# Kernel tuning notes

Measured on AMD Instinct MI355X. Metric: run time of the kernel, lower is better.

## Reference

```python
import jax, jax.numpy as jnp
import numpy as np

HID = 256
POS_FREQ = 10
DIR_FREQ = 4
POS_ENC = 3 * (2 * POS_FREQ + 1)   # 63
DIR_ENC = 3 * (2 * DIR_FREQ + 1)   # 27
N_PTS = 262144


def _posenc(x, num_freq):
    freqs = (2.0 ** jnp.arange(num_freq)).astype(x.dtype)      # [F]
    xf = x[..., None, :] * freqs[:, None]                       # [..., F, D]
    sc = jnp.stack([jnp.sin(xf), jnp.cos(xf)], axis=-2)         # [..., F, 2, D]
    return jnp.concatenate([x, sc.reshape(*x.shape[:-1], -1)], axis=-1)


def _linear_init(key, fan_in, fan_out):
    kw, kb = jax.random.split(key)
    s = 1.0 / np.sqrt(fan_in)
    W = jax.random.uniform(kw, (fan_in, fan_out), jnp.float32, -s, s)
    b = jax.random.uniform(kb, (fan_out,), jnp.float32, -s, s)
    return W, b


def setup_inputs() -> dict:
    key = jax.random.key(0)
    ks = jax.random.split(key, 16)
    inp = {
        "positions": jax.random.normal(ks[0], (N_PTS, 3), jnp.float32),
        "directions": jax.random.normal(ks[1], (N_PTS, 3), jnp.float32),
    }
    W, b = _linear_init(ks[2], POS_ENC, HID)
    inp["W_in"], inp["b_in"] = W, b
    # 7 hidden layers; layer index 4 takes skip concat (HID + POS_ENC)
    for i in range(7):
        fan_in = HID + POS_ENC if i == 4 else HID
        W, b = _linear_init(ks[3 + i], fan_in, HID)
        inp[f"W_h{i}"], inp[f"b_h{i}"] = W, b
    W, b = _linear_init(ks[10], HID, HID + 1)
    inp["W_out"], inp["b_out"] = W, b
    W, b = _linear_init(ks[11], HID + DIR_ENC, HID // 2)
    inp["W_r1"], inp["b_r1"] = W, b
    W, b = _linear_init(ks[12], HID // 2, 3)
    inp["W_r2"], inp["b_r2"] = W, b
    return inp


def _forward(positions, directions, W_in, b_in, hidden_params, W_out, b_out,
             W_r1, b_r1, W_r2, b_r2):
    pe = _posenc(positions, POS_FREQ)    # [N, 63]
    de = _posenc(directions, DIR_FREQ)   # [N, 27]
    h = jax.nn.relu(pe @ W_in + b_in)    # [N, 256]
    for i, (W, b) in enumerate(hidden_params):
        if i == 4:
            h = jnp.concatenate([h, pe], axis=-1)  # skip connection [N, 319]
        h = jax.nn.relu(h @ W + b)
    out = h @ W_out + b_out                      # [N, 257]
    features = out[..., :HID]                    # [N, 256]
    density = jax.nn.relu(out[..., HID:HID + 1])  # [N, 1]
    rgb_in = jnp.concatenate([features, de], axis=-1)  # [N, 283]
    rgb = jax.nn.sigmoid(jax.nn.relu(rgb_in @ W_r1 + b_r1) @ W_r2 + b_r2)  # [N, 3]
    return rgb, density


def reference(positions, directions, W_in, b_in,
              W_h0, b_h0, W_h1, b_h1, W_h2, b_h2, W_h3, b_h3,
              W_h4, b_h4, W_h5, b_h5, W_h6, b_h6,
              W_out, b_out, W_r1, b_r1, W_r2, b_r2):
    hidden = [(W_h0, b_h0), (W_h1, b_h1), (W_h2, b_h2), (W_h3, b_h3),
              (W_h4, b_h4), (W_h5, b_h5), (W_h6, b_h6)]
    return _forward(positions, directions, W_in, b_in, hidden,
                    W_out, b_out, W_r1, b_r1, W_r2, b_r2)
```

## Files before the change

### kernel.cpp

```cpp
#include <hip/hip_runtime.h>
#include <math.h>

#define NPTS 262144
#define MT 64
#define XS 328
#define NWAVE 8

typedef __attribute__((ext_vector_type(8))) short bf16x8;
typedef __attribute__((ext_vector_type(4))) float f32x4;
typedef __attribute__((ext_vector_type(2))) unsigned int u32x2;

__device__ __forceinline__ short f2bf(float f) {
    union { float f; unsigned u; } v; v.f = f;
    unsigned r = v.u + 0x7fffu + ((v.u >> 16) & 1u);
    return (short)(r >> 16);
}
__device__ __forceinline__ unsigned pk2(float a, float b) {
    return ((unsigned)(unsigned short)f2bf(a)) |
           ((unsigned)(unsigned short)f2bf(b) << 16);
}

#define OFF_IN   0
#define SZ_IN    (64*256)
#define OFF_H0   (OFF_IN + SZ_IN)
#define SZ_H     (256*256)
#define OFF_H1   (OFF_H0 + SZ_H)
#define OFF_H2   (OFF_H1 + SZ_H)
#define OFF_H3   (OFF_H2 + SZ_H)
#define OFF_H4   (OFF_H3 + SZ_H)
#define SZ_H4    (320*256)
#define OFF_H5   (OFF_H4 + SZ_H4)
#define OFF_H6   (OFF_H5 + SZ_H)
#define OFF_OUT  (OFF_H6 + SZ_H)
#define SZ_OUT   (256*272)
#define OFF_R1   (OFF_OUT + SZ_OUT)
#define SZ_R1    (288*128)
#define OFF_R2   (OFF_R1 + SZ_R1)
#define SZ_R2    (128*16)
#define WS_TOTAL (OFF_R2 + SZ_R2)

struct PrepP { const float* W[11]; short* ws; };

__global__ __launch_bounds__(256) void prep_all(PrepP pp) {
    int i = blockIdx.x * 256 + threadIdx.x;
    if (i >= WS_TOTAL) return;
    const int offs[12] = {OFF_IN, OFF_H0, OFF_H1, OFF_H2, OFF_H3, OFF_H4,
                          OFF_H5, OFF_H6, OFF_OUT, OFF_R1, OFF_R2, WS_TOTAL};
    const int Ks[11]  = {63,256,256,256,256,319,256,256,256,283,128};
    const int Ns[11]  = {256,256,256,256,256,256,256,256,257,128,3};
    const int Nps[11] = {256,256,256,256,256,256,256,256,272,128,16};
    int seg = 0;
    while (i >= offs[seg + 1]) seg++;
    int li = i - offs[seg];
    int j = li & 7, L = (li >> 3) & 63, tile = li >> 9;
    int nNt = Nps[seg] >> 4;
    int nt = tile % nNt, kt = tile / nNt;
    int k = kt * 32 + ((L >> 4) << 3) + j;
    int n = nt * 16 + (L & 15);
    float v = (k < Ks[seg] && n < Ns[seg]) ? pp.W[seg][k * Ns[seg] + n] : 0.f;
    pp.ws[i] = f2bf(v);
}

struct Params {
    const float *pos, *dir;
    const float *b_in, *b_h0, *b_h1, *b_h2, *b_h3, *b_h4, *b_h5, *b_h6;
    const float *b_out, *b_r1, *b_r2;
    const short *w;
    float *out;
};

template<int NKT, int NS, int NT, int MODE>
__device__ __forceinline__ void layerT(const short* __restrict__ Wsw,
                                       const float* __restrict__ bias,
                                       short* X, float* dout, int p0,
                                       int wave, int lane) {
    const int l15 = lane & 15, quad = lane >> 4;
    f32x4 acc[NS][4];
#pragma unroll
    for (int s = 0; s < NS; s++)
#pragma unroll
        for (int t = 0; t < 4; t++) acc[s][t] = (f32x4){0.f, 0.f, 0.f, 0.f};
    __syncthreads();
    const short* xb = X + l15 * XS + quad * 8;
    for (int kt = 0; kt < NKT; ++kt) {
        bf16x8 b[4];
#pragma unroll
        for (int t = 0; t < 4; t++)
            b[t] = *(const bf16x8*)(xb + t * 16 * XS + kt * 32);
#pragma unroll
        for (int s = 0; s < NS; s++) {
            const int nt = s * NWAVE + wave;
            if (NS * NWAVE > NT && nt >= NT) break;
            bf16x8 a = *(const bf16x8*)(Wsw + (size_t)((kt * NT + nt) * 64 + lane) * 8);
#pragma unroll
            for (int t = 0; t < 4; t++)
                acc[s][t] = __builtin_amdgcn_mfma_f32_16x16x32_bf16(a, b[t], acc[s][t], 0, 0, 0);
        }
    }
    __syncthreads();
#pragma unroll
    for (int s = 0; s < NS; s++) {
        const int nt = s * NWAVE + wave;
        if (NS * NWAVE > NT && nt >= NT) break;
        if (MODE == 1 && nt == 16) {
            if (quad == 0) {
                const float bv = bias[256];
#pragma unroll
                for (int t = 0; t < 4; t++) {
                    const int m = t * 16 + l15;
                    dout[3 * NPTS + p0 + m] = fmaxf(acc[s][t][0] + bv, 0.f);
                }
            }
        } else {
            const int n0 = nt * 16 + quad * 4;
            const f32x4 bv = *(const f32x4*)(bias + n0);
#pragma unroll
            for (int t = 0; t < 4; t++) {
                const int m = t * 16 + l15;
                float v0 = acc[s][t][0] + bv[0];
                float v1 = acc[s][t][1] + bv[1];
                float v2 = acc[s][t][2] + bv[2];
                float v3 = acc[s][t][3] + bv[3];
                if (MODE == 0) {
                    v0 = fmaxf(v0, 0.f); v1 = fmaxf(v1, 0.f);
                    v2 = fmaxf(v2, 0.f); v3 = fmaxf(v3, 0.f);
                }
                u32x2 w; w[0] = pk2(v0, v1); w[1] = pk2(v2, v3);
                *(u32x2*)(X + m * XS + n0) = w;
            }
        }
    }
}

__global__ __launch_bounds__(512, 6) void nerf_fused(Params P) {
    __shared__ __align__(16) short X[MT * XS];
    __shared__ __align__(16) short DE[MT * 32];
    const int tid = threadIdx.x;
    const int wave = tid >> 6, lane = tid & 63;
    const int p0 = blockIdx.x * MT;

    for (int i = tid; i < MT * 64; i += 512) {
        const int pt = i >> 6, d = i & 63;
        float v = 0.f;
        if (d < 3) v = P.pos[(p0 + pt) * 3 + d];
        else if (d < 63) {
            const int e = d - 3, f = e / 6, r = e % 6;
            const float x = P.pos[(p0 + pt) * 3 + (r % 3)];
            const float xf = x * (float)(1 << f);
            v = (r < 3) ? sinf(xf) : cosf(xf);
        }
        const short bv = f2bf(v);
        X[pt * XS + d] = bv;
        X[pt * XS + 256 + d] = bv;
    }
    for (int i = tid; i < MT * 32; i += 512) {
        const int pt = i >> 5, d = i & 31;
        float v = 0.f;
        if (d < 3) v = P.dir[(p0 + pt) * 3 + d];
        else if (d < 27) {
            const int e = d - 3, f = e / 6, r = e % 6;
            const float x = P.dir[(p0 + pt) * 3 + (r % 3)];
            const float xf = x * (float)(1 << f);
            v = (r < 3) ? sinf(xf) : cosf(xf);
        }
        DE[i] = f2bf(v);
    }

    layerT<2, 2, 16, 0>(P.w + OFF_IN, P.b_in, X, P.out, p0, wave, lane);
    layerT<8, 2, 16, 0>(P.w + OFF_H0, P.b_h0, X, P.out, p0, wave, lane);
    layerT<8, 2, 16, 0>(P.w + OFF_H1, P.b_h1, X, P.out, p0, wave, lane);
    layerT<8, 2, 16, 0>(P.w + OFF_H2, P.b_h2, X, P.out, p0, wave, lane);
    layerT<8, 2, 16, 0>(P.w + OFF_H3, P.b_h3, X, P.out, p0, wave, lane);
    layerT<10, 2, 16, 0>(P.w + OFF_H4, P.b_h4, X, P.out, p0, wave, lane);
    layerT<8, 2, 16, 0>(P.w + OFF_H5, P.b_h5, X, P.out, p0, wave, lane);
    layerT<8, 2, 16, 0>(P.w + OFF_H6, P.b_h6, X, P.out, p0, wave, lane);
    layerT<8, 3, 17, 1>(P.w + OFF_OUT, P.b_out, X, P.out, p0, wave, lane);

    __syncthreads();
    for (int i = tid; i < MT * 32; i += 512) {
        const int pt = i >> 5, d = i & 31;
        X[pt * XS + 256 + d] = DE[i];
    }

    layerT<9, 1, 8, 0>(P.w + OFF_R1, P.b_r1, X, P.out, p0, wave, lane);

    __syncthreads();
    if (wave < 4) {
        const int l15 = lane & 15, quad = lane >> 4;
        f32x4 acc = (f32x4){0.f, 0.f, 0.f, 0.f};
        const short* xb = X + (wave * 16 + l15) * XS + quad * 8;
#pragma unroll
        for (int kt = 0; kt < 4; ++kt) {
            bf16x8 b = *(const bf16x8*)(xb + kt * 32);
            bf16x8 a = *(const bf16x8*)(P.w + OFF_R2 + (size_t)(kt * 64 + lane) * 8);
            acc = __builtin_amdgcn_mfma_f32_16x16x32_bf16(a, b, acc, 0, 0, 0);
        }
        if (quad == 0) {
#pragma unroll
            for (int r = 0; r < 3; r++) {
                const float v = acc[r] + P.b_r2[r];
                P.out[(size_t)(p0 + wave * 16 + l15) * 3 + r] = 1.f / (1.f + expf(-v));
            }
        }
    }
}

extern "C" void kernel_launch(void* const* d_in, const int* in_sizes, int n_in,
                              void* d_out, int out_size, void* d_ws, size_t ws_size,
                              hipStream_t stream) {
    short* ws = (short*)d_ws;

    PrepP pp;
    pp.W[0]  = (const float*)d_in[2];
    pp.W[1]  = (const float*)d_in[4];
    pp.W[2]  = (const float*)d_in[6];
    pp.W[3]  = (const float*)d_in[8];
    pp.W[4]  = (const float*)d_in[10];
    pp.W[5]  = (const float*)d_in[12];
    pp.W[6]  = (const float*)d_in[14];
    pp.W[7]  = (const float*)d_in[16];
    pp.W[8]  = (const float*)d_in[18];
    pp.W[9]  = (const float*)d_in[20];
    pp.W[10] = (const float*)d_in[22];
    pp.ws = ws;
    hipLaunchKernelGGL(prep_all, dim3((WS_TOTAL + 255) / 256), dim3(256), 0, stream, pp);

    Params P;
    P.pos  = (const float*)d_in[0];
    P.dir  = (const float*)d_in[1];
    P.b_in = (const float*)d_in[3];
    P.b_h0 = (const float*)d_in[5];
    P.b_h1 = (const float*)d_in[7];
    P.b_h2 = (const float*)d_in[9];
    P.b_h3 = (const float*)d_in[11];
    P.b_h4 = (const float*)d_in[13];
    P.b_h5 = (const float*)d_in[15];
    P.b_h6 = (const float*)d_in[17];
    P.b_out = (const float*)d_in[19];
    P.b_r1 = (const float*)d_in[21];
    P.b_r2 = (const float*)d_in[23];
    P.w = ws;
    P.out = (float*)d_out;
    hipLaunchKernelGGL(nerf_fused, dim3(NPTS / MT), dim3(512), 0, stream, P);
}
```

Measured before the change: 441.9 us.

## Double point tile to 128 with 16 waves and 2D wave tiling

Each block now handles 128 points with 1024 threads, and each wave owns a 4-column-tile by 2-row-tile block of every layer's output instead of striding over N-tiles. Each weight fragment fetched from global memory is therefore reused across twice as many points. The density column of the output layer moves to a separate small MFMA pass run by the first eight waves. LDS becomes dynamic and grows to about 90 KB, so fewer blocks fit per CU, which lowers occupancy and leaves less latency hiding.

```diff
diff --git a/kernel.cpp b/kernel.cpp
--- a/kernel.cpp
+++ b/kernel.cpp
@@ -2,9 +2,9 @@
 #include <math.h>
 
 #define NPTS 262144
-#define MT 64
+#define MT 128
 #define XS 328
-#define NWAVE 8
+#define NTHREADS 1024
 
 typedef __attribute__((ext_vector_type(8))) short bf16x8;
 typedef __attribute__((ext_vector_type(4))) float f32x4;
@@ -69,77 +69,81 @@
     float *out;
 };
 
-template<int NKT, int NS, int NT, int MODE>
+template<int NKT, int NT, int NS, int TM, int MODE>
 __device__ __forceinline__ void layerT(const short* __restrict__ Wsw,
                                        const float* __restrict__ bias,
                                        short* X, float* dout, int p0,
-                                       int wave, int lane) {
+                                       int ntBase, int mtBase, int wave, int lane) {
     const int l15 = lane & 15, quad = lane >> 4;
-    f32x4 acc[NS][4];
-#pragma unroll
-    for (int s = 0; s < NS; s++)
-#pragma unroll
-        for (int t = 0; t < 4; t++) acc[s][t] = (f32x4){0.f, 0.f, 0.f, 0.f};
     __syncthreads();
     const short* xb = X + l15 * XS + quad * 8;
+
+    if (MODE == 1 && wave < 8) {
+        f32x4 ad = (f32x4){0.f, 0.f, 0.f, 0.f};
+        for (int kt = 0; kt < NKT; ++kt) {
+            bf16x8 b = *(const bf16x8*)(xb + wave * 16 * XS + kt * 32);
+            bf16x8 a = *(const bf16x8*)(Wsw + (size_t)((kt * NT + 16) * 64 + lane) * 8);
+            ad = __builtin_amdgcn_mfma_f32_16x16x32_bf16(a, b, ad, 0, 0, 0);
+        }
+        if (quad == 0)
+            dout[3 * NPTS + p0 + wave * 16 + l15] = fmaxf(ad[0] + bias[256], 0.f);
+    }
+
+    f32x4 acc[NS][TM];
+#pragma unroll
+    for (int s = 0; s < NS; s++)
+#pragma unroll
+        for (int t = 0; t < TM; t++) acc[s][t] = (f32x4){0.f, 0.f, 0.f, 0.f};
+
     for (int kt = 0; kt < NKT; ++kt) {
-        bf16x8 b[4];
-#pragma unroll
-        for (int t = 0; t < 4; t++)
-            b[t] = *(const bf16x8*)(xb + t * 16 * XS + kt * 32);
+        bf16x8 b[TM];
+#pragma unroll
+        for (int t = 0; t < TM; t++)
+            b[t] = *(const bf16x8*)(xb + (mtBase + t) * 16 * XS + kt * 32);
 #pragma unroll
         for (int s = 0; s < NS; s++) {
-            const int nt = s * NWAVE + wave;
-            if (NS * NWAVE > NT && nt >= NT) break;
-            bf16x8 a = *(const bf16x8*)(Wsw + (size_t)((kt * NT + nt) * 64 + lane) * 8);
-#pragma unroll
-            for (int t = 0; t < 4; t++)
+            bf16x8 a = *(const bf16x8*)(Wsw + (size_t)((kt * NT + ntBase + s) * 64 + lane) * 8);
+#pragma unroll
+            for (int t = 0; t < TM; t++)
                 acc[s][t] = __builtin_amdgcn_mfma_f32_16x16x32_bf16(a, b[t], acc[s][t], 0, 0, 0);
         }
     }
     __syncthreads();
 #pragma unroll
     for (int s = 0; s < NS; s++) {
-        const int nt = s * NWAVE + wave;
-        if (NS * NWAVE > NT && nt >= NT) break;
-        if (MODE == 1 && nt == 16) {
-            if (quad == 0) {
-                const float bv = bias[256];
-#pragma unroll
-                for (int t = 0; t < 4; t++) {
-                    const int m = t * 16 + l15;
-                    dout[3 * NPTS + p0 + m] = fmaxf(acc[s][t][0] + bv, 0.f);
-                }
+        const int n0 = (ntBase + s) * 16 + quad * 4;
+        const f32x4 bv = *(const f32x4*)(bias + n0);
+#pragma unroll
+        for (int t = 0; t < TM; t++) {
+            const int m = (mtBase + t) * 16 + l15;
+            float v0 = acc[s][t][0] + bv[0];
+            float v1 = acc[s][t][1] + bv[1];
+            float v2 = acc[s][t][2] + bv[2];
+            float v3 = acc[s][t][3] + bv[3];
+            if (MODE == 0) {
+                v0 = fmaxf(v0, 0.f); v1 = fmaxf(v1, 0.f);
+                v2 = fmaxf(v2, 0.f); v3 = fmaxf(v3, 0.f);
             }
-        } else {
-            const int n0 = nt * 16 + quad * 4;
-            const f32x4 bv = *(const f32x4*)(bias + n0);
-#pragma unroll
-            for (int t = 0; t < 4; t++) {
-                const int m = t * 16 + l15;
-                float v0 = acc[s][t][0] + bv[0];
-                float v1 = acc[s][t][1] + bv[1];
-                float v2 = acc[s][t][2] + bv[2];
-                float v3 = acc[s][t][3] + bv[3];
-                if (MODE == 0) {
-                    v0 = fmaxf(v0, 0.f); v1 = fmaxf(v1, 0.f);
-                    v2 = fmaxf(v2, 0.f); v3 = fmaxf(v3, 0.f);
-                }
-                u32x2 w; w[0] = pk2(v0, v1); w[1] = pk2(v2, v3);
-                *(u32x2*)(X + m * XS + n0) = w;
-            }
-        }
-    }
-}
-
-__global__ __launch_bounds__(512, 6) void nerf_fused(Params P) {
-    __shared__ __align__(16) short X[MT * XS];
-    __shared__ __align__(16) short DE[MT * 32];
+            u32x2 w; w[0] = pk2(v0, v1); w[1] = pk2(v2, v3);
+            *(u32x2*)(X + m * XS + n0) = w;
+        }
+    }
+}
+
+__global__ __launch_bounds__(NTHREADS, 4) void nerf_fused(Params P) {
+    extern __shared__ short smem[];
+    short* X = smem;
+    short* DE = smem + MT * XS;
     const int tid = threadIdx.x;
     const int wave = tid >> 6, lane = tid & 63;
     const int p0 = blockIdx.x * MT;
 
-    for (int i = tid; i < MT * 64; i += 512) {
+    const int ntB_h = (wave & 3) * 4;
+    const int mtB_h = (wave >> 2) * 2;
+    const int ntB_r = (wave & 7);
+    const int mtB_r = (wave >> 3) * 4;
+
+    for (int i = tid; i < MT * 64; i += NTHREADS) {
         const int pt = i >> 6, d = i & 63;
         float v = 0.f;
         if (d < 3) v = P.pos[(p0 + pt) * 3 + d];
@@ -153,7 +157,7 @@
         X[pt * XS + d] = bv;
         X[pt * XS + 256 + d] = bv;
     }
-    for (int i = tid; i < MT * 32; i += 512) {
+    for (int i = tid; i < MT * 32; i += NTHREADS) {
         const int pt = i >> 5, d = i & 31;
         float v = 0.f;
         if (d < 3) v = P.dir[(p0 + pt) * 3 + d];
@@ -166,26 +170,25 @@
         DE[i] = f2bf(v);
     }
 
-    layerT<2, 2, 16, 0>(P.w + OFF_IN, P.b_in, X, P.out, p0, wave, lane);
-    layerT<8, 2, 16, 0>(P.w + OFF_H0, P.b_h0, X, P.out, p0, wave, lane);
-    layerT<8, 2, 16, 0>(P.w + OFF_H1, P.b_h1, X, P.out, p0, wave, lane);
-    layerT<8, 2, 16, 0>(P.w + OFF_H2, P.b_h2, X, P.out, p0, wave, lane);
-    layerT<8, 2, 16, 0>(P.w + OFF_H3, P.b_h3, X, P.out, p0, wave, lane);
-    layerT<10, 2, 16, 0>(P.w + OFF_H4, P.b_h4, X, P.out, p0, wave, lane);
-    layerT<8, 2, 16, 0>(P.w + OFF_H5, P.b_h5, X, P.out, p0, wave, lane);
-    layerT<8, 2, 16, 0>(P.w + OFF_H6, P.b_h6, X, P.out, p0, wave, lane);
-    layerT<8, 3, 17, 1>(P.w + OFF_OUT, P.b_out, X, P.out, p0, wave, lane);
-
-    __syncthreads();
-    for (int i = tid; i < MT * 32; i += 512) {
+    layerT<2, 16, 4, 2, 0>(P.w + OFF_IN, P.b_in, X, P.out, p0, ntB_h, mtB_h, wave, lane);
+    layerT<8, 16, 4, 2, 0>(P.w + OFF_H0, P.b_h0, X, P.out, p0, ntB_h, mtB_h, wave, lane);
+    layerT<8, 16, 4, 2, 0>(P.w + OFF_H1, P.b_h1, X, P.out, p0, ntB_h, mtB_h, wave, lane);
+    layerT<8, 16, 4, 2, 0>(P.w + OFF_H2, P.b_h2, X, P.out, p0, ntB_h, mtB_h, wave, lane);
+    layerT<8, 16, 4, 2, 0>(P.w + OFF_H3, P.b_h3, X, P.out, p0, ntB_h, mtB_h, wave, lane);
+    layerT<10, 16, 4, 2, 0>(P.w + OFF_H4, P.b_h4, X, P.out, p0, ntB_h, mtB_h, wave, lane);
+    layerT<8, 16, 4, 2, 0>(P.w + OFF_H5, P.b_h5, X, P.out, p0, ntB_h, mtB_h, wave, lane);
+    layerT<8, 16, 4, 2, 0>(P.w + OFF_H6, P.b_h6, X, P.out, p0, ntB_h, mtB_h, wave, lane);
+    layerT<8, 17, 4, 2, 1>(P.w + OFF_OUT, P.b_out, X, P.out, p0, ntB_h, mtB_h, wave, lane);
+
+    for (int i = tid; i < MT * 32; i += NTHREADS) {
         const int pt = i >> 5, d = i & 31;
         X[pt * XS + 256 + d] = DE[i];
     }
 
-    layerT<9, 1, 8, 0>(P.w + OFF_R1, P.b_r1, X, P.out, p0, wave, lane);
+    layerT<9, 8, 1, 4, 0>(P.w + OFF_R1, P.b_r1, X, P.out, p0, ntB_r, mtB_r, wave, lane);
 
     __syncthreads();
-    if (wave < 4) {
+    if (wave < 8) {
         const int l15 = lane & 15, quad = lane >> 4;
         f32x4 acc = (f32x4){0.f, 0.f, 0.f, 0.f};
         const short* xb = X + (wave * 16 + l15) * XS + quad * 8;
@@ -204,6 +207,8 @@
         }
     }
 }
+
+#define SMEM_BYTES ((MT * XS + MT * 32) * 2)
 
 extern "C" void kernel_launch(void* const* d_in, const int* in_sizes, int n_in,
                               void* d_out, int out_size, void* d_ws, size_t ws_size,
@@ -241,5 +246,8 @@
     P.b_r2 = (const float*)d_in[23];
     P.w = ws;
     P.out = (float*)d_out;
-    hipLaunchKernelGGL(nerf_fused, dim3(NPTS / MT), dim3(512), 0, stream, P);
-}
+
+    (void)hipFuncSetAttribute((const void*)nerf_fused,
+                              hipFuncAttributeMaxDynamicSharedMemorySize, SMEM_BYTES);
+    hipLaunchKernelGGL(nerf_fused, dim3(NPTS / MT), dim3(NTHREADS), SMEM_BYTES, stream, P);
+}
```

Result: slower. 593.6 us (+34.3%).

## Switch MLP layers to 32x32x16 MFMA with 2D wave tiling

Applied to the files above, without the earlier changes.

Replaces the 16x16x32 bf16 MFMA tiling, where each wave covered all 64 rows and 2 column tiles, with 32x32x16 MFMA in which each wave owns a 32-row by 64-column block. The weight prepack layout changes to match 32-wide N tiles and 16-deep K tiles. The extra density column gets its own MFMA pass on two waves. Also uses the hardware packed bf16 convert when it is available. The aim is fewer LDS operand loads per FLOP and higher MFMA throughput, at the cost of larger accumulators per wave and some padded compute for the density and rgb output columns.

```diff
diff --git a/kernel.cpp b/kernel.cpp
--- a/kernel.cpp
+++ b/kernel.cpp
@@ -8,7 +8,14 @@
 
 typedef __attribute__((ext_vector_type(8))) short bf16x8;
 typedef __attribute__((ext_vector_type(4))) float f32x4;
+typedef __attribute__((ext_vector_type(16))) float f32x16;
 typedef __attribute__((ext_vector_type(2))) unsigned int u32x2;
+
+#if defined(__has_builtin)
+#if __has_builtin(__builtin_amdgcn_cvt_pk_bf16_f32)
+#define HAVE_CVT_PK_BF16 1
+#endif
+#endif
 
 __device__ __forceinline__ short f2bf(float f) {
     union { float f; unsigned u; } v; v.f = f;
@@ -16,8 +23,14 @@
     return (short)(r >> 16);
 }
 __device__ __forceinline__ unsigned pk2(float a, float b) {
+#ifdef HAVE_CVT_PK_BF16
+    auto r = __builtin_amdgcn_cvt_pk_bf16_f32(a, b);
+    unsigned u; __builtin_memcpy(&u, &r, 4);
+    return u;
+#else
     return ((unsigned)(unsigned short)f2bf(a)) |
            ((unsigned)(unsigned short)f2bf(b) << 16);
+#endif
 }
 
 #define OFF_IN   0
@@ -32,11 +45,11 @@
 #define OFF_H5   (OFF_H4 + SZ_H4)
 #define OFF_H6   (OFF_H5 + SZ_H)
 #define OFF_OUT  (OFF_H6 + SZ_H)
-#define SZ_OUT   (256*272)
+#define SZ_OUT   (256*288)
 #define OFF_R1   (OFF_OUT + SZ_OUT)
 #define SZ_R1    (288*128)
 #define OFF_R2   (OFF_R1 + SZ_R1)
-#define SZ_R2    (128*16)
+#define SZ_R2    (128*32)
 #define WS_TOTAL (OFF_R2 + SZ_R2)
 
 struct PrepP { const float* W[11]; short* ws; };
@@ -48,15 +61,15 @@
                           OFF_H5, OFF_H6, OFF_OUT, OFF_R1, OFF_R2, WS_TOTAL};
     const int Ks[11]  = {63,256,256,256,256,319,256,256,256,283,128};
     const int Ns[11]  = {256,256,256,256,256,256,256,256,257,128,3};
-    const int Nps[11] = {256,256,256,256,256,256,256,256,272,128,16};
+    const int nNts[11]= {8,8,8,8,8,8,8,8,9,4,1};
     int seg = 0;
     while (i >= offs[seg + 1]) seg++;
     int li = i - offs[seg];
     int j = li & 7, L = (li >> 3) & 63, tile = li >> 9;
-    int nNt = Nps[seg] >> 4;
+    int nNt = nNts[seg];
     int nt = tile % nNt, kt = tile / nNt;
-    int k = kt * 32 + ((L >> 4) << 3) + j;
-    int n = nt * 16 + (L & 15);
+    int k = kt * 16 + ((L >> 5) << 3) + j;
+    int n = nt * 32 + (L & 31);
     float v = (k < Ks[seg] && n < Ns[seg]) ? pp.W[seg][k * Ns[seg] + n] : 0.f;
     pp.ws[i] = f2bf(v);
 }
@@ -69,65 +82,62 @@
     float *out;
 };
 
-template<int NKT, int NS, int NT, int MODE>
+template<int NKT, int NT, int NS, int MODE>
 __device__ __forceinline__ void layerT(const short* __restrict__ Wsw,
                                        const float* __restrict__ bias,
                                        short* X, float* dout, int p0,
-                                       int wave, int lane) {
-    const int l15 = lane & 15, quad = lane >> 4;
-    f32x4 acc[NS][4];
+                                       int ntB, int mt, int wave, int lane) {
+    const int l31 = lane & 31, hi = lane >> 5;
+    __syncthreads();
+
+    if (MODE == 1 && wave < 2) {
+        f32x16 ad;
+#pragma unroll
+        for (int e = 0; e < 16; e++) ad[e] = 0.f;
+        const short* xd = X + (wave * 32 + l31) * XS + hi * 8;
+        for (int kt = 0; kt < NKT; ++kt) {
+            bf16x8 b = *(const bf16x8*)(xd + kt * 16);
+            bf16x8 a = *(const bf16x8*)(Wsw + (size_t)((kt * NT + 8) * 64 + lane) * 8);
+            ad = __builtin_amdgcn_mfma_f32_32x32x16_bf16(a, b, ad, 0, 0, 0);
+        }
+        if (hi == 0)
+            dout[3 * NPTS + p0 + wave * 32 + l31] = fmaxf(ad[0] + bias[256], 0.f);
+    }
+
+    f32x16 acc[NS];
 #pragma unroll
     for (int s = 0; s < NS; s++)
 #pragma unroll
-        for (int t = 0; t < 4; t++) acc[s][t] = (f32x4){0.f, 0.f, 0.f, 0.f};
+        for (int e = 0; e < 16; e++) acc[s][e] = 0.f;
+
+    const short* xb = X + (mt * 32 + l31) * XS + hi * 8;
+    for (int kt = 0; kt < NKT; ++kt) {
+        bf16x8 b = *(const bf16x8*)(xb + kt * 16);
+#pragma unroll
+        for (int s = 0; s < NS; s++) {
+            bf16x8 a = *(const bf16x8*)(Wsw + (size_t)((kt * NT + ntB + s) * 64 + lane) * 8);
+            acc[s] = __builtin_amdgcn_mfma_f32_32x32x16_bf16(a, b, acc[s], 0, 0, 0);
+        }
+    }
     __syncthreads();
-    const short* xb = X + l15 * XS + quad * 8;
-    for (int kt = 0; kt < NKT; ++kt) {
-        bf16x8 b[4];
-#pragma unroll
-        for (int t = 0; t < 4; t++)
-            b[t] = *(const bf16x8*)(xb + t * 16 * XS + kt * 32);
-#pragma unroll
-        for (int s = 0; s < NS; s++) {
-            const int nt = s * NWAVE + wave;
-            if (NS * NWAVE > NT && nt >= NT) break;
-            bf16x8 a = *(const bf16x8*)(Wsw + (size_t)((kt * NT + nt) * 64 + lane) * 8);
-#pragma unroll
-            for (int t = 0; t < 4; t++)
-                acc[s][t] = __builtin_amdgcn_mfma_f32_16x16x32_bf16(a, b[t], acc[s][t], 0, 0, 0);
-        }
-    }
-    __syncthreads();
+    const int p = mt * 32 + l31;
 #pragma unroll
     for (int s = 0; s < NS; s++) {
-        const int nt = s * NWAVE + wave;
-        if (NS * NWAVE > NT && nt >= NT) break;
-        if (MODE == 1 && nt == 16) {
-            if (quad == 0) {
-                const float bv = bias[256];
-#pragma unroll
-                for (int t = 0; t < 4; t++) {
-                    const int m = t * 16 + l15;
-                    dout[3 * NPTS + p0 + m] = fmaxf(acc[s][t][0] + bv, 0.f);
-                }
+        const int nbase = (ntB + s) * 32;
+#pragma unroll
+        for (int c = 0; c < 4; c++) {
+            const int n0 = nbase + 8 * c + 4 * hi;
+            const f32x4 bv = *(const f32x4*)(bias + n0);
+            float v0 = acc[s][c * 4 + 0] + bv[0];
+            float v1 = acc[s][c * 4 + 1] + bv[1];
+            float v2 = acc[s][c * 4 + 2] + bv[2];
+            float v3 = acc[s][c * 4 + 3] + bv[3];
+            if (MODE == 0) {
+                v0 = fmaxf(v0, 0.f); v1 = fmaxf(v1, 0.f);
+                v2 = fmaxf(v2, 0.f); v3 = fmaxf(v3, 0.f);
             }
-        } else {
-            const int n0 = nt * 16 + quad * 4;
-            const f32x4 bv = *(const f32x4*)(bias + n0);
-#pragma unroll
-            for (int t = 0; t < 4; t++) {
-                const int m = t * 16 + l15;
-                float v0 = acc[s][t][0] + bv[0];
-                float v1 = acc[s][t][1] + bv[1];
-                float v2 = acc[s][t][2] + bv[2];
-                float v3 = acc[s][t][3] + bv[3];
-                if (MODE == 0) {
-                    v0 = fmaxf(v0, 0.f); v1 = fmaxf(v1, 0.f);
-                    v2 = fmaxf(v2, 0.f); v3 = fmaxf(v3, 0.f);
-                }
-                u32x2 w; w[0] = pk2(v0, v1); w[1] = pk2(v2, v3);
-                *(u32x2*)(X + m * XS + n0) = w;
-            }
+            u32x2 w; w[0] = pk2(v0, v1); w[1] = pk2(v2, v3);
+            *(u32x2*)(X + p * XS + n0) = w;
         }
     }
 }
@@ -138,6 +148,11 @@
     const int tid = threadIdx.x;
     const int wave = tid >> 6, lane = tid & 63;
     const int p0 = blockIdx.x * MT;
+
+    const int ntB_h = (wave & 3) * 2;
+    const int mt_h  = wave >> 2;
+    const int ntB_r = wave & 3;
+    const int mt_r  = wave >> 2;
 
     for (int i = tid; i < MT * 64; i += 512) {
         const int pt = i >> 6, d = i & 63;
@@ -166,40 +181,41 @@
         DE[i] = f2bf(v);
     }
 
-    layerT<2, 2, 16, 0>(P.w + OFF_IN, P.b_in, X, P.out, p0, wave, lane);
-    layerT<8, 2, 16, 0>(P.w + OFF_H0, P.b_h0, X, P.out, p0, wave, lane);
-    layerT<8, 2, 16, 0>(P.w + OFF_H1, P.b_h1, X, P.out, p0, wave, lane);
-    layerT<8, 2, 16, 0>(P.w + OFF_H2, P.b_h2, X, P.out, p0, wave, lane);
-    layerT<8, 2, 16, 0>(P.w + OFF_H3, P.b_h3, X, P.out, p0, wave, lane);
-    layerT<10, 2, 16, 0>(P.w + OFF_H4, P.b_h4, X, P.out, p0, wave, lane);
-    layerT<8, 2, 16, 0>(P.w + OFF_H5, P.b_h5, X, P.out, p0, wave, lane);
-    layerT<8, 2, 16, 0>(P.w + OFF_H6, P.b_h6, X, P.out, p0, wave, lane);
-    layerT<8, 3, 17, 1>(P.w + OFF_OUT, P.b_out, X, P.out, p0, wave, lane);
-
-    __syncthreads();
+    layerT<4, 8, 2, 0>(P.w + OFF_IN, P.b_in, X, P.out, p0, ntB_h, mt_h, wave, lane);
+    layerT<16, 8, 2, 0>(P.w + OFF_H0, P.b_h0, X, P.out, p0, ntB_h, mt_h, wave, lane);
+    layerT<16, 8, 2, 0>(P.w + OFF_H1, P.b_h1, X, P.out, p0, ntB_h, mt_h, wave, lane);
+    layerT<16, 8, 2, 0>(P.w + OFF_H2, P.b_h2, X, P.out, p0, ntB_h, mt_h, wave, lane);
+    layerT<16, 8, 2, 0>(P.w + OFF_H3, P.b_h3, X, P.out, p0, ntB_h, mt_h, wave, lane);
+    layerT<20, 8, 2, 0>(P.w + OFF_H4, P.b_h4, X, P.out, p0, ntB_h, mt_h, wave, lane);
+    layerT<16, 8, 2, 0>(P.w + OFF_H5, P.b_h5, X, P.out, p0, ntB_h, mt_h, wave, lane);
+    layerT<16, 8, 2, 0>(P.w + OFF_H6, P.b_h6, X, P.out, p0, ntB_h, mt_h, wave, lane);
+    layerT<16, 9, 2, 1>(P.w + OFF_OUT, P.b_out, X, P.out, p0, ntB_h, mt_h, wave, lane);
+
     for (int i = tid; i < MT * 32; i += 512) {
         const int pt = i >> 5, d = i & 31;
         X[pt * XS + 256 + d] = DE[i];
     }
 
-    layerT<9, 1, 8, 0>(P.w + OFF_R1, P.b_r1, X, P.out, p0, wave, lane);
+    layerT<18, 4, 1, 0>(P.w + OFF_R1, P.b_r1, X, P.out, p0, ntB_r, mt_r, wave, lane);
 
     __syncthreads();
-    if (wave < 4) {
-        const int l15 = lane & 15, quad = lane >> 4;
-        f32x4 acc = (f32x4){0.f, 0.f, 0.f, 0.f};
-        const short* xb = X + (wave * 16 + l15) * XS + quad * 8;
-#pragma unroll
-        for (int kt = 0; kt < 4; ++kt) {
-            bf16x8 b = *(const bf16x8*)(xb + kt * 32);
+    if (wave < 2) {
+        const int l31 = lane & 31, hi = lane >> 5;
+        f32x16 acc;
+#pragma unroll
+        for (int e = 0; e < 16; e++) acc[e] = 0.f;
+        const short* xb = X + (wave * 32 + l31) * XS + hi * 8;
+#pragma unroll
+        for (int kt = 0; kt < 8; ++kt) {
+            bf16x8 b = *(const bf16x8*)(xb + kt * 16);
             bf16x8 a = *(const bf16x8*)(P.w + OFF_R2 + (size_t)(kt * 64 + lane) * 8);
-            acc = __builtin_amdgcn_mfma_f32_16x16x32_bf16(a, b, acc, 0, 0, 0);
-        }
-        if (quad == 0) {
+            acc = __builtin_amdgcn_mfma_f32_32x32x16_bf16(a, b, acc, 0, 0, 0);
+        }
+        if (hi == 0) {
 #pragma unroll
             for (int r = 0; r < 3; r++) {
                 const float v = acc[r] + P.b_r2[r];
-                P.out[(size_t)(p0 + wave * 16 + l15) * 3 + r] = 1.f / (1.f + expf(-v));
+                P.out[(size_t)(p0 + wave * 32 + l31) * 3 + r] = 1.f / (1.f + expf(-v));
             }
         }
     }
```

Measured after the change: 659.2 us. 1.49x slower.
